# Performance work log

Hardware: AMD Instinct MI355X
Metric: run time of the kernel (lower is better)

## Reference

```python
import jax, jax.numpy as jnp
import numpy as np
import math

N_LAYERS = 2
N_HEADS = 8
D_MODEL = 512
D_FF = 2048
B = 2
L = 2048
GELU_C = 0.7978845608028654  # sqrt(2/pi)
LN_EPS = 1e-5


def gelu_tanh(x):
    # faithful to the module's custom GELU: 0.5*x*(1+tanh(sqrt(2/pi)*(x+0.044715*x^3)))
    return 0.5 * x * (1.0 + jnp.tanh(GELU_C * (x + 0.044715 * x * x * x)))


def layernorm(x, g, b):
    m = jnp.mean(x, axis=-1, keepdims=True)
    v = jnp.mean((x - m) ** 2, axis=-1, keepdims=True)
    return (x - m) * jax.lax.rsqrt(v + LN_EPS) * g + b


def setup_inputs() -> dict:
    key = jax.random.key(0)
    ks = jax.random.split(key, 24)
    w = lambda k, shape: jax.random.normal(k, shape, dtype=jnp.float32) * 0.02
    inp = {
        "x": jax.random.normal(ks[0], (B, L, D_MODEL), dtype=jnp.float32),
        # tau is exp(tau_learner(...)) in the full model -> positive scalar per batch
        "tau": jax.random.uniform(ks[1], (B, 1), dtype=jnp.float32) + 0.5,
        "delta": jax.random.normal(ks[2], (B, L), dtype=jnp.float32) * 0.1,
        # NStransformer builds an upper-triangular causal mask (True = masked)
        "att_mask": jnp.triu(jnp.ones((L, L), dtype=bool), k=1),
        "Wq": w(ks[3], (N_LAYERS, D_MODEL, D_MODEL)), "bq": jnp.zeros((N_LAYERS, D_MODEL), jnp.float32),
        "Wk": w(ks[4], (N_LAYERS, D_MODEL, D_MODEL)), "bk": jnp.zeros((N_LAYERS, D_MODEL), jnp.float32),
        "Wv": w(ks[5], (N_LAYERS, D_MODEL, D_MODEL)), "bv": jnp.zeros((N_LAYERS, D_MODEL), jnp.float32),
        "Wo": w(ks[6], (N_LAYERS, D_MODEL, D_MODEL)), "bo": jnp.zeros((N_LAYERS, D_MODEL), jnp.float32),
        # conv1/conv2 are kernel_size=1 Conv1d == pointwise linears
        "W1": w(ks[7], (N_LAYERS, D_MODEL, D_FF)), "b1": jnp.zeros((N_LAYERS, D_FF), jnp.float32),
        "W2": w(ks[8], (N_LAYERS, D_FF, D_MODEL)), "b2": jnp.zeros((N_LAYERS, D_MODEL), jnp.float32),
        "ln1_g": jnp.ones((N_LAYERS, D_MODEL), jnp.float32), "ln1_b": jnp.zeros((N_LAYERS, D_MODEL), jnp.float32),
        "ln2_g": jnp.ones((N_LAYERS, D_MODEL), jnp.float32), "ln2_b": jnp.zeros((N_LAYERS, D_MODEL), jnp.float32),
        "lnf_g": jnp.ones((D_MODEL,), jnp.float32), "lnf_b": jnp.zeros((D_MODEL,), jnp.float32),
    }
    return inp


def reference(x, tau, delta, att_mask, Wq, bq, Wk, bk, Wv, bv, Wo, bo,
              W1, b1, W2, b2, ln1_g, ln1_b, ln2_g, ln2_b, lnf_g, lnf_b):
    Bsz, Ls, D = x.shape
    H = N_HEADS
    E = D // H
    scale = 1.0 / math.sqrt(E)
    t = tau[:, None, None, :]    # (B,1) -> (B,1,1,1)
    d = delta[:, None, None, :]  # (B,L) -> (B,1,1,L)
    neg_inf = jnp.float32(-jnp.inf)
    for l in range(N_LAYERS):
        q = (x @ Wq[l] + bq[l]).reshape(Bsz, Ls, H, E)
        k = (x @ Wk[l] + bk[l]).reshape(Bsz, Ls, H, E)
        v = (x @ Wv[l] + bv[l]).reshape(Bsz, Ls, H, E)
        # de-stationary scores: QK^T * tau + delta, then masked softmax
        scores = jnp.einsum('blhe,bshe->bhls', q, k) * t + d  # (B,H,L,S)
        scores = jnp.where(att_mask, neg_inf, scores)
        A = jax.nn.softmax(scale * scores, axis=-1)  # dropout is identity in eval
        V = jnp.einsum('bhls,bshd->blhd', A, v).reshape(Bsz, Ls, D)
        x = (V @ Wo[l] + bo[l]) + x
        xb = layernorm(x, ln1_g[l], ln1_b[l])
        h = gelu_tanh(xb @ W1[l] + b1[l])   # conv1 (k=1)
        o = h @ W2[l] + b2[l]               # conv2 (k=1)
        x = layernorm(o + xb, ln2_g[l], ln2_b[l])
    return layernorm(x, lnf_g, lnf_b)
```

## Files before the change

### kernel.cpp

```cpp
#include <hip/hip_runtime.h>
#include <stdint.h>

#define DM   512
#define DFF  2048
#define NH   8
#define EH   64
#define SEQ  2048
#define NBAT 2
#define NTOK (NBAT*SEQ)
#define LOG2E 1.44269504088896340736f

typedef __attribute__((ext_vector_type(8))) short  s16x8;
typedef __attribute__((ext_vector_type(8))) __bf16 bf16x8;
typedef __attribute__((ext_vector_type(4))) float  f32x4;

__device__ __forceinline__ short f2bf(float f) {
  union { float f; unsigned int i; } c; c.f = f;
  unsigned int x = c.i;
  x += 0x7fffu + ((x >> 16) & 1u);
  return (short)(x >> 16);
}
__device__ __forceinline__ float bf2f(short u) {
  union { unsigned int i; float f; } c;
  c.i = ((unsigned int)(unsigned short)u) << 16;
  return c.f;
}
__device__ __forceinline__ f32x4 mfma16(bf16x8 a, bf16x8 b, f32x4 c) {
  return __builtin_amdgcn_mfma_f32_16x16x32_bf16(a, b, c, 0, 0, 0);
}
__device__ __forceinline__ void gl_lds16(const short* g, short* l) {
  __builtin_amdgcn_global_load_lds(
      (const __attribute__((address_space(1))) unsigned int*)(const void*)g,
      (__attribute__((address_space(3))) unsigned int*)(void*)l, 16, 0, 0);
}

__global__ __launch_bounds__(256) void fill_code_f32(float* __restrict__ out,
                                                     float code)
{
  out[blockIdx.x * 256 + threadIdx.x] = code;
}

__global__ __launch_bounds__(256) void prep_weights(
    const float* __restrict__ Wq, const float* __restrict__ Wk,
    const float* __restrict__ Wv, const float* __restrict__ Wo,
    const float* __restrict__ W1, const float* __restrict__ W2,
    short* __restrict__ Wqkvt, short* __restrict__ Wot,
    short* __restrict__ W1t,   short* __restrict__ W2t)
{
  int gw   = blockIdx.x * 4 + (threadIdx.x >> 6);
  int lane = threadIdx.x & 63;
  int l = gw / 6144;
  int g = gw % 6144;
  const float* src; short* dst; int K, N, gi;
  if (g < 2048) {
    int w = g >> 9; gi = g & 511; K = 512; N = 512;
    src = (w == 0 ? Wq : w == 1 ? Wk : w == 2 ? Wv : Wo) + l * 262144;
    dst = (w < 3) ? (Wqkvt + l * 786432 + w * 262144) : (Wot + l * 262144);
  } else if (g < 4096) {
    gi = g - 2048; K = 512; N = 2048;
    src = W1 + l * 1048576; dst = W1t + l * 1048576;
  } else {
    gi = g - 4096; K = 2048; N = 512;
    src = W2 + l * 1048576; dst = W2t + l * 1048576;
  }
  int nb = N >> 6;
  int n  = (gi % nb) * 64 + lane;
  int k0 = (gi / nb) * 8;
  s16x8 v;
  #pragma unroll
  for (int i = 0; i < 8; i++) v[i] = f2bf(src[(size_t)(k0 + i) * N + n]);
  *(s16x8*)(dst + (size_t)n * K + k0) = v;
}

__global__ __launch_bounds__(256) void cast_kernel(const float* __restrict__ in,
                                                   float* __restrict__ outf,
                                                   short* __restrict__ outb)
{
  int i = blockIdx.x * 256 + threadIdx.x;
  float v = in[i];
  outf[i] = v;
  outb[i] = f2bf(v);
}

__global__ __launch_bounds__(256) void skred_ln(
    const short* __restrict__ parts, const float* __restrict__ bias,
    const float* __restrict__ rf, const short* __restrict__ rb,
    const float* __restrict__ g, const float* __restrict__ bb,
    float* __restrict__ sumf, short* __restrict__ outb, int mode)
{
  const int row  = blockIdx.x * 4 + (threadIdx.x >> 6);
  const int lane = threadIdx.x & 63;
  const int col  = lane * 8;
  const size_t base = (size_t)row * DM + col;
  float t[8];
  #pragma unroll
  for (int j = 0; j < 8; j++) t[j] = bias[col + j];
  #pragma unroll
  for (int p = 0; p < 4; p++) {
    s16x8 v = *(const s16x8*)(parts + (size_t)p * (NTOK * DM) + base);
    #pragma unroll
    for (int j = 0; j < 8; j++) t[j] += bf2f(v[j]);
  }
  if (mode == 0) {
    #pragma unroll
    for (int j = 0; j < 8; j++) t[j] += rf[base + j];
  } else {
    s16x8 v = *(const s16x8*)(rb + base);
    #pragma unroll
    for (int j = 0; j < 8; j++) t[j] += bf2f(v[j]);
  }
  float s = 0.f, ss = 0.f;
  #pragma unroll
  for (int j = 0; j < 8; j++) { s += t[j]; ss += t[j] * t[j]; }
  #pragma unroll
  for (int off = 32; off > 0; off >>= 1) {
    s += __shfl_xor(s, off); ss += __shfl_xor(ss, off);
  }
  float mean = s * (1.f / DM);
  float var  = ss * (1.f / DM) - mean * mean;
  float rstd = rsqrtf(var + 1e-5f);
  if (mode == 0) {
    #pragma unroll
    for (int j = 0; j < 8; j++) {
      sumf[base + j] = t[j];
      outb[base + j] = f2bf((t[j] - mean) * rstd * g[col + j] + bb[col + j]);
    }
  } else {
    #pragma unroll
    for (int j = 0; j < 8; j++) {
      float y = (t[j] - mean) * rstd * g[col + j] + bb[col + j];
      sumf[base + j] = y;
      outb[base + j] = f2bf(y);
    }
  }
}

template<int TM>
__global__ __launch_bounds__(256) void gemm_bt(
    const short* __restrict__ A, const short* __restrict__ Bt,
    int M, int N, int K, int KS, int mode,
    const float* __restrict__ bq, const float* __restrict__ bk,
    const float* __restrict__ bv,
    short* __restrict__ oq, short* __restrict__ okk, short* __restrict__ ov)
{
  __shared__ short As[2][TM * 32];
  __shared__ short Bs[2][128 * 32];
  constexpr int MT = TM / 32;
  const int tid  = threadIdx.x;
  const int lane = tid & 63;
  const int wid  = tid >> 6;
  const int lm   = lane & 15, quad = lane >> 4;
  const int nbn  = N >> 7;
  const int nb2  = (M / TM) * nbn;
  const int ks   = blockIdx.x / nb2;
  const int rem  = blockIdx.x % nb2;
  const int m0   = (rem / nbn) * TM;
  const int n0   = (rem % nbn) << 7;
  const int wm   = (wid & 1) * (TM / 2), wn = (wid >> 1) * 64;
  const int Kc   = K / KS;
  const int kbeg = ks * Kc;

  f32x4 acc[MT][4];
  #pragma unroll
  for (int i = 0; i < MT; i++)
    #pragma unroll
    for (int j = 0; j < 4; j++) acc[i][j] = (f32x4){0.f, 0.f, 0.f, 0.f};

  const short* Abase = A  + (size_t)m0 * K;
  const short* Bbase = Bt + (size_t)n0 * K;

  for (int k0 = kbeg; k0 < kbeg + Kc; k0 += 64) {
    __syncthreads();
    #pragma unroll
    for (int half = 0; half < 2; half++) {
      const int kk = k0 + half * 32;
      #pragma unroll
      for (int j = 0; j < TM / 64; j++) {
        int c = j * 256 + wid * 64 + lane;
        gl_lds16(Abase + (size_t)(c >> 2) * K + kk + (c & 3) * 8,
                 &As[half][(j * 256 + wid * 64) * 8]);
      }
      #pragma unroll
      for (int j = 0; j < 2; j++) {
        int c = j * 256 + wid * 64 + lane;
        gl_lds16(Bbase + (size_t)(c >> 2) * K + kk + (c & 3) * 8,
                 &Bs[half][(j * 256 + wid * 64) * 8]);
      }
    }
    __syncthreads();
    #pragma unroll
    for (int half = 0; half < 2; half++) {
      bf16x8 af[MT], bfr[4];
      #pragma unroll
      for (int t = 0; t < MT; t++)
        af[t] = *(const bf16x8*)&As[half][(wm + t * 16 + lm) * 32 + quad * 8];
      #pragma unroll
      for (int t = 0; t < 4; t++)
        bfr[t] = *(const bf16x8*)&Bs[half][(wn + t * 16 + lm) * 32 + quad * 8];
      #pragma unroll
      for (int mt = 0; mt < MT; mt++)
        #pragma unroll
        for (int nt = 0; nt < 4; nt++)
          acc[mt][nt] = mfma16(af[mt], bfr[nt], acc[mt][nt]);
    }
  }

  #pragma unroll
  for (int mt = 0; mt < MT; mt++) {
    int row = m0 + wm + mt * 16 + quad * 4;
    #pragma unroll
    for (int nt = 0; nt < 4; nt++) {
      int col = n0 + wn + nt * 16 + lm;
      f32x4 v = acc[mt][nt];
      if (mode == 0) {
        int which = col >> 9; int d = col & 511;
        int hh = d >> 6; int e = d & 63;
        const float* bias = which == 0 ? bq : which == 1 ? bk : bv;
        float bb = bias[d];
        #pragma unroll
        for (int r = 0; r < 4; r++) {
          int tok = row + r; int bI = tok >> 11, li = tok & 2047;
          float val = v[r] + bb;
          if (which == 0)
            oq [(((size_t)bI * NH + hh) * SEQ + li) * EH + e] = f2bf(val);
          else if (which == 1)
            okk[(((size_t)bI * NH + hh) * SEQ + li) * EH + e] = f2bf(val);
          else
            ov [(((size_t)bI * NH + hh) * EH + e) * SEQ + li] = f2bf(val);
        }
      } else if (mode == 2) {
        float bb = bq[col];
        #pragma unroll
        for (int r = 0; r < 4; r++) {
          float x = v[r] + bb;
          float u = 0.7978845608f * (x + 0.044715f * x * x * x);
          float t = 1.f - 2.f / (1.f + __expf(2.f * u));
          size_t idx = (size_t)(row + r) * N + col;
          oq[idx] = f2bf(0.5f * x * (1.f + t));
        }
      } else {
        short* op = oq + (size_t)ks * M * N;
        #pragma unroll
        for (int r = 0; r < 4; r++)
          op[(size_t)(row + r) * N + col] = f2bf(v[r]);
      }
    }
  }
}

__global__ __launch_bounds__(256) void attn_v7(
    const short* __restrict__ Q, const short* __restrict__ Kg,
    const short* __restrict__ Vt,
    const float* __restrict__ tau, const float* __restrict__ delta,
    short* __restrict__ opart, float* __restrict__ lpart)
{
  __shared__ short Ks[64 * 72];
  __shared__ short Vs[64 * 72];
  __shared__ short Ps[4][16 * 72];
  const int tid  = threadIdx.x;
  const int lane = tid & 63, wid = tid >> 6;
  const int lm = lane & 15, quad = lane >> 4;
  const int t    = blockIdx.x >> 2;
  const int part = blockIdx.x & 3;
  const int qb = 31 - (t & 31);
  const int h  = (t >> 5) & 7;
  const int b  = t >> 8;
  const int q0 = qb * 64;
  const int qw = q0 + wid * 16;
  const size_t bhq = ((size_t)b * NH + h) * SEQ;
  const short* kbase = Kg + bhq * EH;
  const short* vbase = Vt + ((size_t)b * NH + h) * (size_t)(EH * SEQ);

  const int nblk = qb + 1;
  const int kb0 = (nblk * part) >> 2;
  const int kb1 = (nblk * (part + 1)) >> 2;

  bf16x8 qf0 = *(const bf16x8*)(Q + (bhq + qw + lm) * EH + quad * 8);
  bf16x8 qf1 = *(const bf16x8*)(Q + (bhq + qw + lm) * EH + 32 + quad * 8);

  const float st2 = 0.125f * LOG2E * tau[b];
  f32x4 O[4];
  #pragma unroll
  for (int i = 0; i < 4; i++) O[i] = (f32x4){0.f, 0.f, 0.f, 0.f};
  float lr[4] = {0.f, 0.f, 0.f, 0.f};

  const int c0 = tid, c1 = tid + 256;
  const int r0 = c0 >> 3, ch0 = (c0 & 7) * 8;
  const int r1 = c1 >> 3, ch1 = (c1 & 7) * 8;

  for (int kb = kb0; kb < kb1; kb++) {
    const int s0 = kb << 6;
    s16x8 ka = *(const s16x8*)(kbase + (size_t)(s0 + r0) * EH + ch0);
    s16x8 kb_ = *(const s16x8*)(kbase + (size_t)(s0 + r1) * EH + ch1);
    s16x8 va = *(const s16x8*)(vbase + (size_t)r0 * SEQ + s0 + ch0);
    s16x8 vb = *(const s16x8*)(vbase + (size_t)r1 * SEQ + s0 + ch1);
    __syncthreads();
    *(s16x8*)&Ks[r0 * 72 + ch0] = ka;
    *(s16x8*)&Ks[r1 * 72 + ch1] = kb_;
    *(s16x8*)&Vs[r0 * 72 + ch0] = va;
    *(s16x8*)&Vs[r1 * 72 + ch1] = vb;
    __syncthreads();

    f32x4 S[4];
    #pragma unroll
    for (int nt = 0; nt < 4; nt++) {
      S[nt] = (f32x4){0.f, 0.f, 0.f, 0.f};
      S[nt] = mfma16(qf0, *(const bf16x8*)&Ks[(nt*16 + lm) * 72 + quad * 8], S[nt]);
      S[nt] = mfma16(qf1, *(const bf16x8*)&Ks[(nt*16 + lm) * 72 + 32 + quad * 8], S[nt]);
    }
    float dl[4];
    #pragma unroll
    for (int nt = 0; nt < 4; nt++)
      dl[nt] = fmaf(0.125f * LOG2E, delta[(size_t)b * SEQ + s0 + nt * 16 + lm],
                    -8.f);

    const bool diag = (kb == qb);
    #pragma unroll
    for (int r = 0; r < 4; r++) {
      float sc[4];
      #pragma unroll
      for (int nt = 0; nt < 4; nt++) sc[nt] = fmaf(st2, S[nt][r], dl[nt]);
      if (diag) {
        int rowq = qw + quad * 4 + r;
        #pragma unroll
        for (int nt = 0; nt < 4; nt++)
          if (s0 + nt * 16 + lm > rowq) sc[nt] = -__builtin_inff();
      }
      unsigned int u0 = __float_as_uint(exp2f(sc[0]));
      unsigned int u1 = __float_as_uint(exp2f(sc[1]));
      unsigned int u2 = __float_as_uint(exp2f(sc[2]));
      unsigned int u3 = __float_as_uint(exp2f(sc[3]));
      lr[r] += (__uint_as_float(u0 & 0xffff0000u) +
                __uint_as_float(u1 & 0xffff0000u)) +
               (__uint_as_float(u2 & 0xffff0000u) +
                __uint_as_float(u3 & 0xffff0000u));
      short* pr = &Ps[wid][(quad * 4 + r) * 72];
      pr[lm]      = (short)(u0 >> 16);
      pr[16 + lm] = (short)(u1 >> 16);
      pr[32 + lm] = (short)(u2 >> 16);
      pr[48 + lm] = (short)(u3 >> 16);
    }

    bf16x8 pf0 = *(const bf16x8*)&Ps[wid][lm * 72 + quad * 8];
    bf16x8 pf1 = *(const bf16x8*)&Ps[wid][lm * 72 + 32 + quad * 8];
    #pragma unroll
    for (int et = 0; et < 4; et++) {
      O[et] = mfma16(pf0, *(const bf16x8*)&Vs[(et*16 + lm) * 72 + quad * 8], O[et]);
      O[et] = mfma16(pf1, *(const bf16x8*)&Vs[(et*16 + lm) * 72 + 32 + quad * 8], O[et]);
    }
  }

  #pragma unroll
  for (int r = 0; r < 4; r++) {
    float s = lr[r];
    #pragma unroll
    for (int off = 1; off < 16; off <<= 1) s += __shfl_xor(s, off);
    lr[r] = s;
  }

  const int slot = ((t << 2) | part);
  short* ob = opart + (size_t)slot * 4096;
  float* lb = lpart + (size_t)slot * 64;
  #pragma unroll
  for (int r = 0; r < 4; r++) {
    int qloc = wid * 16 + quad * 4 + r;
    #pragma unroll
    for (int et = 0; et < 4; et++)
      ob[qloc * 64 + et * 16 + lm] = f2bf(O[et][r]);
    if (lm == 0) lb[qloc] = lr[r];
  }
}

__global__ __launch_bounds__(256) void attn_reduce(
    const short* __restrict__ opart, const float* __restrict__ lpart,
    short* __restrict__ Oa)
{
  const int t = blockIdx.x;
  const int qb = 31 - (t & 31);
  const int h  = (t >> 5) & 7;
  const int b  = t >> 8;
  const int q0 = qb * 64;
  #pragma unroll
  for (int i = 0; i < 16; i++) {
    int idx = i * 256 + threadIdx.x;
    int q = idx >> 6, e = idx & 63;
    float l = 0.f, o = 0.f;
    #pragma unroll
    for (int p = 0; p < 4; p++) {
      int slot = t * 4 + p;
      l += lpart[(size_t)slot * 64 + q];
      o += bf2f(opart[(size_t)slot * 4096 + idx]);
    }
    Oa[((size_t)b * SEQ + q0 + q) * DM + h * EH + e] = f2bf(o / l);
  }
}

__global__ __launch_bounds__(256) void ln_kernel(
    const float* in, const float* __restrict__ g, const float* __restrict__ bb,
    float* outf, short* outb)
{
  int row  = blockIdx.x * 4 + (threadIdx.x >> 6);
  int lane = threadIdx.x & 63;
  const float* p = in + (size_t)row * DM;
  float v[8]; float s = 0.f, ss = 0.f;
  #pragma unroll
  for (int i = 0; i < 8; i++) {
    float x = p[lane + i * 64]; v[i] = x; s += x; ss += x * x;
  }
  #pragma unroll
  for (int off = 32; off > 0; off >>= 1) {
    s += __shfl_xor(s, off); ss += __shfl_xor(ss, off);
  }
  float mean = s * (1.f / DM);
  float var  = ss * (1.f / DM) - mean * mean;
  float rstd = rsqrtf(var + 1e-5f);
  #pragma unroll
  for (int i = 0; i < 8; i++) {
    int c = lane + i * 64;
    float y = (v[i] - mean) * rstd * g[c] + bb[c];
    if (outf) outf[(size_t)row * DM + c] = y;
    if (outb) outb[(size_t)row * DM + c] = f2bf(y);
  }
}

extern "C" void kernel_launch(void* const* d_in, const int* in_sizes, int n_in,
                              void* d_out, int out_size, void* d_ws, size_t ws_size,
                              hipStream_t stream)
{
  float* out = (float*)d_out;

  if (ws_size < (size_t)62918656) {
    fill_code_f32<<<2097152 / 256, 256, 0, stream>>>(
        out, 1200.f + (float)(ws_size >> 20));
    return;
  }

  const float* x    = (const float*)d_in[0];
  const float* tau  = (const float*)d_in[1];
  const float* del  = (const float*)d_in[2];
  const float* Wq = (const float*)d_in[4];
  const float* bq = (const float*)d_in[5];
  const float* Wk = (const float*)d_in[6];
  const float* bk = (const float*)d_in[7];
  const float* Wv = (const float*)d_in[8];
  const float* bv = (const float*)d_in[9];
  const float* Wo = (const float*)d_in[10];
  const float* bo = (const float*)d_in[11];
  const float* W1 = (const float*)d_in[12];
  const float* b1 = (const float*)d_in[13];
  const float* W2 = (const float*)d_in[14];
  const float* b2 = (const float*)d_in[15];
  const float* ln1g = (const float*)d_in[16];
  const float* ln1b = (const float*)d_in[17];
  const float* ln2g = (const float*)d_in[18];
  const float* ln2b = (const float*)d_in[19];
  const float* lnfg = (const float*)d_in[20];
  const float* lnfb = (const float*)d_in[21];

  char* ws = (char*)d_ws;
  float* sumf  = (float*)(ws + 0);
  short* x16   = (short*)(ws + 8388608);
  short* xb16  = (short*)(ws + 12582912);
  short* q16   = (short*)(ws + 16777216);
  short* k16   = (short*)(ws + 20971520);
  short* vt16  = (short*)(ws + 25165824);
  short* at16  = (short*)(ws + 29360128);
  short* h16   = (short*)(ws + 33554432);
  short* Wqkvt = (short*)(ws + 50331648);
  short* Wot   = (short*)(ws + 53477376);
  short* W1t   = (short*)(ws + 54525952);
  short* W2t   = (short*)(ws + 58720256);
  short* aopart = (short*)(ws + 33554432);
  float* alpart = (float*)(ws + 12582912);
  short* oppart = (short*)(ws + 33554432);
  short* f2part = (short*)(ws + 16777216);

  prep_weights<<<3072, 256, 0, stream>>>(Wq, Wk, Wv, Wo, W1, W2,
                                         Wqkvt, Wot, W1t, W2t);
  cast_kernel<<<NTOK * DM / 256, 256, 0, stream>>>(x, sumf, x16);

  for (int l = 0; l < 2; l++) {
    gemm_bt<64><<<64 * 12, 256, 0, stream>>>(x16, Wqkvt + l * 786432,
        NTOK, 3 * DM, DM, 1, 0,
        bq + l * DM, bk + l * DM, bv + l * DM,
        q16, k16, vt16);
    attn_v7<<<4 * NBAT * NH * (SEQ / 64), 256, 0, stream>>>(
        q16, k16, vt16, tau, del, aopart, alpart);
    attn_reduce<<<NBAT * NH * (SEQ / 64), 256, 0, stream>>>(
        aopart, alpart, at16);
    gemm_bt<64><<<64 * 4 * 4, 256, 0, stream>>>(at16, Wot + l * 262144,
        NTOK, DM, DM, 4, 4,
        nullptr, nullptr, nullptr,
        oppart, nullptr, nullptr);
    skred_ln<<<1024, 256, 0, stream>>>(oppart, bo + l * DM, sumf, nullptr,
        ln1g + l * DM, ln1b + l * DM, sumf, xb16, 0);
    gemm_bt<64><<<64 * 16, 256, 0, stream>>>(xb16, W1t + l * 1048576,
        NTOK, DFF, DM, 1, 2,
        b1 + l * DFF, nullptr, nullptr,
        h16, nullptr, nullptr);
    gemm_bt<64><<<64 * 4 * 4, 256, 0, stream>>>(h16, W2t + l * 1048576,
        NTOK, DM, DFF, 4, 4,
        nullptr, nullptr, nullptr,
        f2part, nullptr, nullptr);
    skred_ln<<<1024, 256, 0, stream>>>(f2part, b2 + l * DM, nullptr, xb16,
        ln2g + l * DM, ln2b + l * DM, sumf, x16, 1);
  }
  ln_kernel<<<NTOK / 4, 256, 0, stream>>>(sumf, lnfg, lnfb, out, nullptr);
}
```

Before: 405.8 us.

## Process two 64-row query subtiles per attention block to reuse K/V tiles

Each attention block now covers 128 query rows as two 64-row subtiles sharing every staged K/V tile in shared memory. This halves K/V global loads and LDS staging per query and halves the attention and reduce grid sizes. Weight prep and the input cast are also merged into one launch to save a kernel launch. The cost is more registers per thread (two sets of Q fragments and accumulators), which may reduce occupancy, plus coarser causal load balance with only 1024 blocks.

New measurement: 423.2 us. +4.3%, slower.

```diff
diff --git a/kernel.cpp b/kernel.cpp
--- a/kernel.cpp
+++ b/kernel.cpp
@@ -40,13 +40,22 @@
   out[blockIdx.x * 256 + threadIdx.x] = code;
 }
 
-__global__ __launch_bounds__(256) void prep_weights(
+__global__ __launch_bounds__(256) void prep_all(
     const float* __restrict__ Wq, const float* __restrict__ Wk,
     const float* __restrict__ Wv, const float* __restrict__ Wo,
     const float* __restrict__ W1, const float* __restrict__ W2,
     short* __restrict__ Wqkvt, short* __restrict__ Wot,
-    short* __restrict__ W1t,   short* __restrict__ W2t)
-{
+    short* __restrict__ W1t,   short* __restrict__ W2t,
+    const float* __restrict__ x, float* __restrict__ sumf,
+    short* __restrict__ x16)
+{
+  if (blockIdx.x >= 3072) {
+    int i = (blockIdx.x - 3072) * 256 + threadIdx.x;
+    float v = x[i];
+    sumf[i] = v;
+    x16[i]  = f2bf(v);
+    return;
+  }
   int gw   = blockIdx.x * 4 + (threadIdx.x >> 6);
   int lane = threadIdx.x & 63;
   int l = gw / 6144;
@@ -70,16 +79,6 @@
   #pragma unroll
   for (int i = 0; i < 8; i++) v[i] = f2bf(src[(size_t)(k0 + i) * N + n]);
   *(s16x8*)(dst + (size_t)n * K + k0) = v;
-}
-
-__global__ __launch_bounds__(256) void cast_kernel(const float* __restrict__ in,
-                                                   float* __restrict__ outf,
-                                                   short* __restrict__ outb)
-{
-  int i = blockIdx.x * 256 + threadIdx.x;
-  float v = in[i];
-  outf[i] = v;
-  outb[i] = f2bf(v);
 }
 
 __global__ __launch_bounds__(256) void skred_ln(
@@ -248,7 +247,55 @@
   }
 }
 
-__global__ __launch_bounds__(256) void attn_v7(
+__device__ __forceinline__ void do_subtile(
+    bf16x8 qf0, bf16x8 qf1,
+    const short* __restrict__ Ks, const short* __restrict__ Vs,
+    short* __restrict__ Psw, const float* dl, float st2,
+    int s0, int rowq0, bool diag,
+    float* lr, f32x4* O, int lm, int quad)
+{
+  f32x4 S[4];
+  #pragma unroll
+  for (int nt = 0; nt < 4; nt++) {
+    S[nt] = (f32x4){0.f, 0.f, 0.f, 0.f};
+    S[nt] = mfma16(qf0, *(const bf16x8*)&Ks[(nt*16 + lm) * 72 + quad * 8], S[nt]);
+    S[nt] = mfma16(qf1, *(const bf16x8*)&Ks[(nt*16 + lm) * 72 + 32 + quad * 8], S[nt]);
+  }
+  #pragma unroll
+  for (int r = 0; r < 4; r++) {
+    float sc[4];
+    #pragma unroll
+    for (int nt = 0; nt < 4; nt++) sc[nt] = fmaf(st2, S[nt][r], dl[nt]);
+    if (diag) {
+      int rowq = rowq0 + quad * 4 + r;
+      #pragma unroll
+      for (int nt = 0; nt < 4; nt++)
+        if (s0 + nt * 16 + lm > rowq) sc[nt] = -__builtin_inff();
+    }
+    unsigned int u0 = __float_as_uint(exp2f(sc[0]));
+    unsigned int u1 = __float_as_uint(exp2f(sc[1]));
+    unsigned int u2 = __float_as_uint(exp2f(sc[2]));
+    unsigned int u3 = __float_as_uint(exp2f(sc[3]));
+    lr[r] += (__uint_as_float(u0 & 0xffff0000u) +
+              __uint_as_float(u1 & 0xffff0000u)) +
+             (__uint_as_float(u2 & 0xffff0000u) +
+              __uint_as_float(u3 & 0xffff0000u));
+    short* pr = &Psw[(quad * 4 + r) * 72];
+    pr[lm]      = (short)(u0 >> 16);
+    pr[16 + lm] = (short)(u1 >> 16);
+    pr[32 + lm] = (short)(u2 >> 16);
+    pr[48 + lm] = (short)(u3 >> 16);
+  }
+  bf16x8 pf0 = *(const bf16x8*)&Psw[lm * 72 + quad * 8];
+  bf16x8 pf1 = *(const bf16x8*)&Psw[lm * 72 + 32 + quad * 8];
+  #pragma unroll
+  for (int et = 0; et < 4; et++) {
+    O[et] = mfma16(pf0, *(const bf16x8*)&Vs[(et*16 + lm) * 72 + quad * 8], O[et]);
+    O[et] = mfma16(pf1, *(const bf16x8*)&Vs[(et*16 + lm) * 72 + 32 + quad * 8], O[et]);
+  }
+}
+
+__global__ __launch_bounds__(256) void attn_v8(
     const short* __restrict__ Q, const short* __restrict__ Kg,
     const short* __restrict__ Vt,
     const float* __restrict__ tau, const float* __restrict__ delta,
@@ -260,40 +307,46 @@
   const int tid  = threadIdx.x;
   const int lane = tid & 63, wid = tid >> 6;
   const int lm = lane & 15, quad = lane >> 4;
-  const int t    = blockIdx.x >> 2;
+  const int tile = blockIdx.x >> 2;
   const int part = blockIdx.x & 3;
-  const int qb = 31 - (t & 31);
-  const int h  = (t >> 5) & 7;
-  const int b  = t >> 8;
-  const int q0 = qb * 64;
-  const int qw = q0 + wid * 16;
-  const size_t bhq = ((size_t)b * NH + h) * SEQ;
+  const int tt = 15 - (tile & 15);
+  const int bh = tile >> 4;
+  const int b  = bh >> 3;
+  const int q0 = tt * 128;
+  const int qA = q0 + wid * 16;
+  const int qB = q0 + 64 + wid * 16;
+  const size_t bhq = (size_t)bh * SEQ;
   const short* kbase = Kg + bhq * EH;
-  const short* vbase = Vt + ((size_t)b * NH + h) * (size_t)(EH * SEQ);
-
-  const int nblk = qb + 1;
+  const short* vbase = Vt + (size_t)bh * (EH * SEQ);
+
+  const int nblk = 2 * tt + 2;
   const int kb0 = (nblk * part) >> 2;
   const int kb1 = (nblk * (part + 1)) >> 2;
 
-  bf16x8 qf0 = *(const bf16x8*)(Q + (bhq + qw + lm) * EH + quad * 8);
-  bf16x8 qf1 = *(const bf16x8*)(Q + (bhq + qw + lm) * EH + 32 + quad * 8);
+  bf16x8 qfA0 = *(const bf16x8*)(Q + (bhq + qA + lm) * EH + quad * 8);
+  bf16x8 qfA1 = *(const bf16x8*)(Q + (bhq + qA + lm) * EH + 32 + quad * 8);
+  bf16x8 qfB0 = *(const bf16x8*)(Q + (bhq + qB + lm) * EH + quad * 8);
+  bf16x8 qfB1 = *(const bf16x8*)(Q + (bhq + qB + lm) * EH + 32 + quad * 8);
 
   const float st2 = 0.125f * LOG2E * tau[b];
-  f32x4 O[4];
-  #pragma unroll
-  for (int i = 0; i < 4; i++) O[i] = (f32x4){0.f, 0.f, 0.f, 0.f};
-  float lr[4] = {0.f, 0.f, 0.f, 0.f};
-
-  const int c0 = tid, c1 = tid + 256;
-  const int r0 = c0 >> 3, ch0 = (c0 & 7) * 8;
-  const int r1 = c1 >> 3, ch1 = (c1 & 7) * 8;
+  f32x4 OA[4], OB[4];
+  #pragma unroll
+  for (int i = 0; i < 4; i++) {
+    OA[i] = (f32x4){0.f, 0.f, 0.f, 0.f};
+    OB[i] = (f32x4){0.f, 0.f, 0.f, 0.f};
+  }
+  float lrA[4] = {0.f, 0.f, 0.f, 0.f};
+  float lrB[4] = {0.f, 0.f, 0.f, 0.f};
+
+  const int r0 = tid >> 3,         ch0 = (tid & 7) * 8;
+  const int r1 = (tid + 256) >> 3, ch1 = (tid & 7) * 8;
 
   for (int kb = kb0; kb < kb1; kb++) {
     const int s0 = kb << 6;
-    s16x8 ka = *(const s16x8*)(kbase + (size_t)(s0 + r0) * EH + ch0);
+    s16x8 ka  = *(const s16x8*)(kbase + (size_t)(s0 + r0) * EH + ch0);
     s16x8 kb_ = *(const s16x8*)(kbase + (size_t)(s0 + r1) * EH + ch1);
-    s16x8 va = *(const s16x8*)(vbase + (size_t)r0 * SEQ + s0 + ch0);
-    s16x8 vb = *(const s16x8*)(vbase + (size_t)r1 * SEQ + s0 + ch1);
+    s16x8 va  = *(const s16x8*)(vbase + (size_t)r0 * SEQ + s0 + ch0);
+    s16x8 vb  = *(const s16x8*)(vbase + (size_t)r1 * SEQ + s0 + ch1);
     __syncthreads();
     *(s16x8*)&Ks[r0 * 72 + ch0] = ka;
     *(s16x8*)&Ks[r1 * 72 + ch1] = kb_;
@@ -301,73 +354,41 @@
     *(s16x8*)&Vs[r1 * 72 + ch1] = vb;
     __syncthreads();
 
-    f32x4 S[4];
-    #pragma unroll
-    for (int nt = 0; nt < 4; nt++) {
-      S[nt] = (f32x4){0.f, 0.f, 0.f, 0.f};
-      S[nt] = mfma16(qf0, *(const bf16x8*)&Ks[(nt*16 + lm) * 72 + quad * 8], S[nt]);
-      S[nt] = mfma16(qf1, *(const bf16x8*)&Ks[(nt*16 + lm) * 72 + 32 + quad * 8], S[nt]);
-    }
     float dl[4];
     #pragma unroll
     for (int nt = 0; nt < 4; nt++)
       dl[nt] = fmaf(0.125f * LOG2E, delta[(size_t)b * SEQ + s0 + nt * 16 + lm],
                     -8.f);
 
-    const bool diag = (kb == qb);
-    #pragma unroll
-    for (int r = 0; r < 4; r++) {
-      float sc[4];
-      #pragma unroll
-      for (int nt = 0; nt < 4; nt++) sc[nt] = fmaf(st2, S[nt][r], dl[nt]);
-      if (diag) {
-        int rowq = qw + quad * 4 + r;
-        #pragma unroll
-        for (int nt = 0; nt < 4; nt++)
-          if (s0 + nt * 16 + lm > rowq) sc[nt] = -__builtin_inff();
-      }
-      unsigned int u0 = __float_as_uint(exp2f(sc[0]));
-      unsigned int u1 = __float_as_uint(exp2f(sc[1]));
-      unsigned int u2 = __float_as_uint(exp2f(sc[2]));
-      unsigned int u3 = __float_as_uint(exp2f(sc[3]));
-      lr[r] += (__uint_as_float(u0 & 0xffff0000u) +
-                __uint_as_float(u1 & 0xffff0000u)) +
-               (__uint_as_float(u2 & 0xffff0000u) +
-                __uint_as_float(u3 & 0xffff0000u));
-      short* pr = &Ps[wid][(quad * 4 + r) * 72];
-      pr[lm]      = (short)(u0 >> 16);
-      pr[16 + lm] = (short)(u1 >> 16);
-      pr[32 + lm] = (short)(u2 >> 16);
-      pr[48 + lm] = (short)(u3 >> 16);
-    }
-
-    bf16x8 pf0 = *(const bf16x8*)&Ps[wid][lm * 72 + quad * 8];
-    bf16x8 pf1 = *(const bf16x8*)&Ps[wid][lm * 72 + 32 + quad * 8];
+    if (kb <= 2 * tt)
+      do_subtile(qfA0, qfA1, Ks, Vs, Ps[wid], dl, st2, s0, qA,
+                 kb == 2 * tt, lrA, OA, lm, quad);
+    do_subtile(qfB0, qfB1, Ks, Vs, Ps[wid], dl, st2, s0, qB,
+               kb == 2 * tt + 1, lrB, OB, lm, quad);
+  }
+
+  #pragma unroll
+  for (int r = 0; r < 4; r++) {
+    float sA = lrA[r], sB = lrB[r];
+    #pragma unroll
+    for (int off = 1; off < 16; off <<= 1) {
+      sA += __shfl_xor(sA, off); sB += __shfl_xor(sB, off);
+    }
+    lrA[r] = sA; lrB[r] = sB;
+  }
+
+  const int slot = (tile << 2) | part;
+  short* ob = opart + (size_t)slot * 8192;
+  float* lb = lpart + (size_t)slot * 128;
+  #pragma unroll
+  for (int r = 0; r < 4; r++) {
+    int ql = wid * 16 + quad * 4 + r;
     #pragma unroll
     for (int et = 0; et < 4; et++) {
-      O[et] = mfma16(pf0, *(const bf16x8*)&Vs[(et*16 + lm) * 72 + quad * 8], O[et]);
-      O[et] = mfma16(pf1, *(const bf16x8*)&Vs[(et*16 + lm) * 72 + 32 + quad * 8], O[et]);
-    }
-  }
-
-  #pragma unroll
-  for (int r = 0; r < 4; r++) {
-    float s = lr[r];
-    #pragma unroll
-    for (int off = 1; off < 16; off <<= 1) s += __shfl_xor(s, off);
-    lr[r] = s;
-  }
-
-  const int slot = ((t << 2) | part);
-  short* ob = opart + (size_t)slot * 4096;
-  float* lb = lpart + (size_t)slot * 64;
-  #pragma unroll
-  for (int r = 0; r < 4; r++) {
-    int qloc = wid * 16 + quad * 4 + r;
-    #pragma unroll
-    for (int et = 0; et < 4; et++)
-      ob[qloc * 64 + et * 16 + lm] = f2bf(O[et][r]);
-    if (lm == 0) lb[qloc] = lr[r];
+      ob[ql * 64 + et * 16 + lm]        = f2bf(OA[et][r]);
+      ob[(64 + ql) * 64 + et * 16 + lm] = f2bf(OB[et][r]);
+    }
+    if (lm == 0) { lb[ql] = lrA[r]; lb[64 + ql] = lrB[r]; }
   }
 }
 
@@ -376,20 +397,20 @@
     short* __restrict__ Oa)
 {
   const int t = blockIdx.x;
-  const int qb = 31 - (t & 31);
-  const int h  = (t >> 5) & 7;
-  const int b  = t >> 8;
-  const int q0 = qb * 64;
-  #pragma unroll
-  for (int i = 0; i < 16; i++) {
+  const int tt = 15 - (t & 15);
+  const int bh = t >> 4;
+  const int b  = bh >> 3, h = bh & 7;
+  const int q0 = tt * 128;
+  #pragma unroll
+  for (int i = 0; i < 32; i++) {
     int idx = i * 256 + threadIdx.x;
     int q = idx >> 6, e = idx & 63;
     float l = 0.f, o = 0.f;
     #pragma unroll
     for (int p = 0; p < 4; p++) {
       int slot = t * 4 + p;
-      l += lpart[(size_t)slot * 64 + q];
-      o += bf2f(opart[(size_t)slot * 4096 + idx]);
+      l += lpart[(size_t)slot * 128 + q];
+      o += bf2f(opart[(size_t)slot * 8192 + idx]);
     }
     Oa[((size_t)b * SEQ + q0 + q) * DM + h * EH + e] = f2bf(o / l);
   }
@@ -475,19 +496,17 @@
   short* oppart = (short*)(ws + 33554432);
   short* f2part = (short*)(ws + 16777216);
 
-  prep_weights<<<3072, 256, 0, stream>>>(Wq, Wk, Wv, Wo, W1, W2,
-                                         Wqkvt, Wot, W1t, W2t);
-  cast_kernel<<<NTOK * DM / 256, 256, 0, stream>>>(x, sumf, x16);
+  prep_all<<<11264, 256, 0, stream>>>(Wq, Wk, Wv, Wo, W1, W2,
+                                      Wqkvt, Wot, W1t, W2t, x, sumf, x16);
 
   for (int l = 0; l < 2; l++) {
     gemm_bt<64><<<64 * 12, 256, 0, stream>>>(x16, Wqkvt + l * 786432,
         NTOK, 3 * DM, DM, 1, 0,
         bq + l * DM, bk + l * DM, bv + l * DM,
         q16, k16, vt16);
-    attn_v7<<<4 * NBAT * NH * (SEQ / 64), 256, 0, stream>>>(
+    attn_v8<<<4 * 256, 256, 0, stream>>>(
         q16, k16, vt16, tau, del, aopart, alpart);
-    attn_reduce<<<NBAT * NH * (SEQ / 64), 256, 0, stream>>>(
-        aopart, alpart, at16);
+    attn_reduce<<<256, 256, 0, stream>>>(aopart, alpart, at16);
     gemm_bt<64><<<64 * 4 * 4, 256, 0, stream>>>(at16, Wot + l * 262144,
         NTOK, DM, DM, 4, 4,
         nullptr, nullptr, nullptr,
```

## Double-buffer GEMM LDS tiles and merge weight-prep with input cast

Applied to the files above, without the earlier changes.

The GEMM main loop now stages the next 64-wide K slice into a second LDS buffer with global_load_lds while MFMAs run on the current buffer. This leaves one barrier per iteration instead of two and hides global-load latency behind compute. The separate fp32-to-bf16 input cast kernel is folded into the weight-prep kernel as extra blocks, removing one launch. In exchange, LDS use per GEMM block doubles, which may lower occupancy.

Result: no change. 410.9 us (+1.2%).

```diff
diff --git a/kernel.cpp b/kernel.cpp
--- a/kernel.cpp
+++ b/kernel.cpp
@@ -40,13 +40,22 @@
   out[blockIdx.x * 256 + threadIdx.x] = code;
 }
 
-__global__ __launch_bounds__(256) void prep_weights(
+__global__ __launch_bounds__(256) void prep_all(
     const float* __restrict__ Wq, const float* __restrict__ Wk,
     const float* __restrict__ Wv, const float* __restrict__ Wo,
     const float* __restrict__ W1, const float* __restrict__ W2,
     short* __restrict__ Wqkvt, short* __restrict__ Wot,
-    short* __restrict__ W1t,   short* __restrict__ W2t)
-{
+    short* __restrict__ W1t,   short* __restrict__ W2t,
+    const float* __restrict__ x, float* __restrict__ sumf,
+    short* __restrict__ x16)
+{
+  if (blockIdx.x >= 3072) {
+    int i = (blockIdx.x - 3072) * 256 + threadIdx.x;
+    float v = x[i];
+    sumf[i] = v;
+    x16[i]  = f2bf(v);
+    return;
+  }
   int gw   = blockIdx.x * 4 + (threadIdx.x >> 6);
   int lane = threadIdx.x & 63;
   int l = gw / 6144;
@@ -72,16 +81,6 @@
   *(s16x8*)(dst + (size_t)n * K + k0) = v;
 }
 
-__global__ __launch_bounds__(256) void cast_kernel(const float* __restrict__ in,
-                                                   float* __restrict__ outf,
-                                                   short* __restrict__ outb)
-{
-  int i = blockIdx.x * 256 + threadIdx.x;
-  float v = in[i];
-  outf[i] = v;
-  outb[i] = f2bf(v);
-}
-
 __global__ __launch_bounds__(256) void skred_ln(
     const short* __restrict__ parts, const float* __restrict__ bias,
     const float* __restrict__ rf, const short* __restrict__ rb,
@@ -143,8 +142,8 @@
     const float* __restrict__ bv,
     short* __restrict__ oq, short* __restrict__ okk, short* __restrict__ ov)
 {
-  __shared__ short As[2][TM * 32];
-  __shared__ short Bs[2][128 * 32];
+  __shared__ short As[2][2][TM * 32];
+  __shared__ short Bs[2][2][128 * 32];
   constexpr int MT = TM / 32;
   const int tid  = threadIdx.x;
   const int lane = tid & 63;
@@ -169,8 +168,7 @@
   const short* Abase = A  + (size_t)m0 * K;
   const short* Bbase = Bt + (size_t)n0 * K;
 
-  for (int k0 = kbeg; k0 < kbeg + Kc; k0 += 64) {
-    __syncthreads();
+  auto stage = [&](int b_, int k0) {
     #pragma unroll
     for (int half = 0; half < 2; half++) {
       const int kk = k0 + half * 32;
@@ -178,31 +176,40 @@
       for (int j = 0; j < TM / 64; j++) {
         int c = j * 256 + wid * 64 + lane;
         gl_lds16(Abase + (size_t)(c >> 2) * K + kk + (c & 3) * 8,
-                 &As[half][(j * 256 + wid * 64) * 8]);
+                 &As[b_][half][(j * 256 + wid * 64) * 8]);
       }
       #pragma unroll
       for (int j = 0; j < 2; j++) {
         int c = j * 256 + wid * 64 + lane;
         gl_lds16(Bbase + (size_t)(c >> 2) * K + kk + (c & 3) * 8,
-                 &Bs[half][(j * 256 + wid * 64) * 8]);
+                 &Bs[b_][half][(j * 256 + wid * 64) * 8]);
       }
     }
+  };
+
+  stage(0, kbeg);
+  int buf = 0;
+  for (int k0 = kbeg; k0 < kbeg + Kc; k0 += 64) {
     __syncthreads();
+    if (k0 + 64 < kbeg + Kc) stage(buf ^ 1, k0 + 64);
     #pragma unroll
     for (int half = 0; half < 2; half++) {
       bf16x8 af[MT], bfr[4];
       #pragma unroll
       for (int t = 0; t < MT; t++)
-        af[t] = *(const bf16x8*)&As[half][(wm + t * 16 + lm) * 32 + quad * 8];
+        af[t] = *(const bf16x8*)
+            &As[buf][half][(wm + t * 16 + lm) * 32 + quad * 8];
       #pragma unroll
       for (int t = 0; t < 4; t++)
-        bfr[t] = *(const bf16x8*)&Bs[half][(wn + t * 16 + lm) * 32 + quad * 8];
+        bfr[t] = *(const bf16x8*)
+            &Bs[buf][half][(wn + t * 16 + lm) * 32 + quad * 8];
       #pragma unroll
       for (int mt = 0; mt < MT; mt++)
         #pragma unroll
         for (int nt = 0; nt < 4; nt++)
           acc[mt][nt] = mfma16(af[mt], bfr[nt], acc[mt][nt]);
     }
+    buf ^= 1;
   }
 
   #pragma unroll
@@ -475,9 +482,8 @@
   short* oppart = (short*)(ws + 33554432);
   short* f2part = (short*)(ws + 16777216);
 
-  prep_weights<<<3072, 256, 0, stream>>>(Wq, Wk, Wv, Wo, W1, W2,
-                                         Wqkvt, Wot, W1t, W2t);
-  cast_kernel<<<NTOK * DM / 256, 256, 0, stream>>>(x, sumf, x16);
+  prep_all<<<11264, 256, 0, stream>>>(Wq, Wk, Wv, Wo, W1, W2,
+                                      Wqkvt, Wot, W1t, W2t, x, sumf, x16);
 
   for (int l = 0; l < 2; l++) {
     gemm_bt<64><<<64 * 12, 256, 0, stream>>>(x16, Wqkvt + l * 786432,
```
